# Performance work log

Hardware: AMD Instinct MI355X
Metric: run time of the kernel (lower is better)

The kernel has to match this reference:

```python
import jax, jax.numpy as jnp
import numpy as np

EPS = 1e-12  # tf.math.l2_normalize epsilon

def _l2norm(x):
    # normalize over last axis, matching K.l2_normalize semantics
    sq = jnp.sum(x * x, axis=-1, keepdims=True)
    return x * jax.lax.rsqrt(jnp.maximum(sq, EPS))

def setup_inputs() -> dict:
    key = jax.random.key(0)
    k1, k2, k3 = jax.random.split(key, 3)
    B, L, D, P = 16, 256, 256, 20
    sent1 = jax.random.normal(k1, (B, L, D), dtype=jnp.float32)
    sent2 = jax.random.normal(k2, (B, L, D), dtype=jnp.float32)
    # glorot_uniform for shape (P, D)
    limit = np.sqrt(6.0 / (P + D)).astype(np.float32)
    kernel = jax.random.uniform(k3, (P, D), minval=-limit, maxval=limit, dtype=jnp.float32)
    return {"sent1": sent1, "sent2": sent2, "kernel": kernel}

def reference(sent1, sent2, kernel):
    # sent1: [B,L1,D], sent2: [B,L2,D], kernel: [P,D]
    v1 = _l2norm(sent1[:, :, None, :] * kernel)  # [B,L1,P,D]
    v2 = _l2norm(sent2[:, :, None, :] * kernel)  # [B,L2,P,D]
    # per-perspective cosine similarity matrix: [B,L1,L2,P]
    cos = jnp.einsum('blpd,bmpd->blmp', v1, v2)
    # max over the other sentence's positions (L2) -> [B,L1,P]
    return jnp.max(cos, axis=2)
```

## Files before the change

### kernel.cpp

```cpp
#include <hip/hip_runtime.h>
#include <hip/hip_bf16.h>


#define B_DIM 16
#define L_DIM 256
#define D_DIM 256
#define P_DIM 20
#define EPS 1e-12f
#define LDP 264

typedef __attribute__((ext_vector_type(8))) __bf16 bf16x8;
typedef __attribute__((ext_vector_type(4))) float f32x4;

__device__ __forceinline__ unsigned short f2bf(float x) {
  unsigned int u = __float_as_uint(x);
  u += 0x7fffu + ((u >> 16) & 1u);
  return (unsigned short)(u >> 16);
}

__global__ __launch_bounds__(256)
void prep2(const float* __restrict__ s1, const float* __restrict__ s2,
           const float* __restrict__ kg,
           float* __restrict__ rn1, float* __restrict__ rn2,
           unsigned short* __restrict__ s1bf, unsigned short* __restrict__ s2bf) {
  __shared__ __align__(16) unsigned short QA[32 * LDP];
  __shared__ __align__(16) unsigned short QB[32 * LDP];
  const int tid = threadIdx.x, lane = tid & 63, wave = tid >> 6;
  const int lr = lane & 15, q = lane >> 4;
  const int sent = blockIdx.x & 1, t = blockIdx.x >> 1;
  const int r0 = t * 32, b = r0 >> 8;
  const float* src = sent ? s2 : s1;
  unsigned short* sbf = sent ? s2bf : s1bf;
  float* rn = sent ? rn2 : rn1;

  #pragma unroll
  for (int i = 0; i < 8; ++i) {
    const int row = i * 4 + wave;
    float4 sv = *(const float4*)(src + (size_t)(r0 + row) * D_DIM + lane * 4);
    unsigned int c0 = ((unsigned int)f2bf(sv.y) << 16) | f2bf(sv.x);
    unsigned int c1 = ((unsigned int)f2bf(sv.w) << 16) | f2bf(sv.z);
    *(uint2*)&sbf[(size_t)(r0 + row) * D_DIM + lane * 4] = make_uint2(c0, c1);
    unsigned int q0 = ((unsigned int)f2bf(sv.y * sv.y) << 16) | f2bf(sv.x * sv.x);
    unsigned int q1 = ((unsigned int)f2bf(sv.w * sv.w) << 16) | f2bf(sv.z * sv.z);
    *(uint2*)&QA[row * LDP + lane * 4] = make_uint2(q0, q1);
  }
  #pragma unroll
  for (int j = 0; j < 5; ++j) {
    const int row = wave * 5 + j;
    float4 kv = *(const float4*)(kg + row * D_DIM + lane * 4);
    unsigned int c0 = ((unsigned int)f2bf(kv.y * kv.y) << 16) | f2bf(kv.x * kv.x);
    unsigned int c1 = ((unsigned int)f2bf(kv.w * kv.w) << 16) | f2bf(kv.z * kv.z);
    *(uint2*)&QB[row * LDP + lane * 4] = make_uint2(c0, c1);
  }
  __syncthreads();

  const int mt = wave & 1, nt = wave >> 1;
  f32x4 acc = {0.f, 0.f, 0.f, 0.f};
  #pragma unroll
  for (int ks = 0; ks < 8; ++ks) {
    const int cc = ks * 4 + q;
    bf16x8 a  = *(const bf16x8*)&QA[(mt * 16 + lr) * LDP + cc * 8];
    bf16x8 bb = *(const bf16x8*)&QB[(nt * 16 + lr) * LDP + cc * 8];
    acc = __builtin_amdgcn_mfma_f32_16x16x32_bf16(a, bb, acc, 0, 0, 0);
  }
  const int p = nt * 16 + lr;
  if (p < P_DIM) {
    #pragma unroll
    for (int r = 0; r < 4; ++r) {
      const int l = (r0 & 255) + mt * 16 + q * 4 + r;
      rn[((size_t)b * P_DIM + p) * L_DIM + l] = rsqrtf(fmaxf(acc[r], EPS));
    }
  }
}

__global__ __launch_bounds__(512, 1)
void mpm_main(const unsigned short* __restrict__ s1bf,
              const unsigned short* __restrict__ s2bf,
              const float* __restrict__ kg, const float* __restrict__ rn1,
              const float* __restrict__ rn2, float* __restrict__ outg) {
  __shared__ __align__(16) unsigned short X2[256 * 256];
  __shared__ __align__(16) unsigned short X1[64 * 256];
  float* WoutF = (float*)X1;

  const int tid = threadIdx.x, lane = tid & 63, wave = tid >> 6;
  const int lr = lane & 15, q = lane >> 4;
  const int bid = blockIdx.x;
  const int pgi = bid & 3, lt = (bid >> 2) & 3, b = bid >> 4;
  const int l0 = lt * 64;

  {
    const unsigned short* s2b = s2bf + (size_t)b * L_DIM * D_DIM;
    #pragma unroll
    for (int j = 0; j < 16; ++j) {
      int g = j * 512 + tid;
      int r = g >> 5, pr = g & 31;
      int c = pr ^ (r & 31);
      __builtin_amdgcn_global_load_lds(
          (const __attribute__((address_space(1))) void*)(s2b + r * 256 + c * 8),
          (__attribute__((address_space(3))) void*)(X2 + (size_t)g * 8), 16, 0, 0);
    }
  }

  uint2 s1r[8];
  {
    const unsigned short* s1b = s1bf + ((size_t)b * L_DIM + l0) * D_DIM;
    #pragma unroll
    for (int i = 0; i < 8; ++i)
      s1r[i] = *(const uint2*)(s1b + (size_t)(i * 8 + wave) * D_DIM + lane * 4);
  }

  const int mrow0 = wave * 32 + lr,  mrow1 = wave * 32 + 16 + lr;
  const int mkey0 = mrow0 & 31,      mkey1 = mrow1 & 31;

  #pragma unroll 1
  for (int pp = 0; pp < 5; ++pp) {
    const int p = pgi * 5 + pp;
    __syncthreads();

    {
      float4 kv = *(const float4*)(kg + p * D_DIM + lane * 4);
      const float k0 = kv.x * kv.x, k1 = kv.y * kv.y, k2 = kv.z * kv.z, k3 = kv.w * kv.w;
      const float* rn1b = rn1 + ((size_t)b * P_DIM + p) * L_DIM + l0;
      #pragma unroll
      for (int i = 0; i < 8; ++i) {
        const int row = i * 8 + wave;
        const float rv = rn1b[row];
        float x0 = __uint_as_float(s1r[i].x << 16)          * k0 * rv;
        float x1 = __uint_as_float(s1r[i].x & 0xffff0000u)  * k1 * rv;
        float x2 = __uint_as_float(s1r[i].y << 16)          * k2 * rv;
        float x3 = __uint_as_float(s1r[i].y & 0xffff0000u)  * k3 * rv;
        unsigned int c0 = ((unsigned int)f2bf(x1) << 16) | f2bf(x0);
        unsigned int c1 = ((unsigned int)f2bf(x3) << 16) | f2bf(x2);
        *(uint2*)&X1[row * 256 + (((lane >> 1) ^ (row & 31)) << 3) + ((lane & 1) << 2)] =
            make_uint2(c0, c1);
      }
    }
    __syncthreads();

    f32x4 acc[2][4];
    #pragma unroll
    for (int mi = 0; mi < 2; ++mi)
      #pragma unroll
      for (int li = 0; li < 4; ++li) acc[mi][li] = (f32x4){0.f, 0.f, 0.f, 0.f};

    #pragma unroll
    for (int ks = 0; ks < 8; ++ks) {
      const int cc = ks * 4 + q;
      bf16x8 a0 = *(const bf16x8*)&X2[mrow0 * 256 + ((cc ^ mkey0) << 3)];
      bf16x8 a1 = *(const bf16x8*)&X2[mrow1 * 256 + ((cc ^ mkey1) << 3)];
      bf16x8 bb[4];
      #pragma unroll
      for (int li = 0; li < 4; ++li) {
        const int l = li * 16 + lr;
        bb[li] = *(const bf16x8*)&X1[l * 256 + ((cc ^ (l & 31)) << 3)];
      }
      #pragma unroll
      for (int li = 0; li < 4; ++li) {
        acc[0][li] = __builtin_amdgcn_mfma_f32_16x16x32_bf16(a0, bb[li], acc[0][li], 0, 0, 0);
        acc[1][li] = __builtin_amdgcn_mfma_f32_16x16x32_bf16(a1, bb[li], acc[1][li], 0, 0, 0);
      }
    }

    float4 r20, r21;
    {
      const float* rn2b = rn2 + ((size_t)b * P_DIM + p) * L_DIM + wave * 32;
      r20 = *(const float4*)(rn2b + q * 4);
      r21 = *(const float4*)(rn2b + 16 + q * 4);
    }
    float v[4];
    #pragma unroll
    for (int li = 0; li < 4; ++li) {
      float t = -3.4e38f;
      t = fmaxf(t, fmaxf(acc[0][li][0] * r20.x, acc[1][li][0] * r21.x));
      t = fmaxf(t, fmaxf(acc[0][li][1] * r20.y, acc[1][li][1] * r21.y));
      t = fmaxf(t, fmaxf(acc[0][li][2] * r20.z, acc[1][li][2] * r21.z));
      t = fmaxf(t, fmaxf(acc[0][li][3] * r20.w, acc[1][li][3] * r21.w));
      t = fmaxf(t, __shfl_xor(t, 16));
      t = fmaxf(t, __shfl_xor(t, 32));
      v[li] = t;
    }

    __syncthreads();
    if (q == 0) {
      #pragma unroll
      for (int li = 0; li < 4; ++li) WoutF[wave * 64 + li * 16 + lr] = v[li];
    }
    __syncthreads();
    if (tid < 64) {
      float o = WoutF[tid];
      #pragma unroll
      for (int w = 1; w < 8; ++w) o = fmaxf(o, WoutF[w * 64 + tid]);
      outg[((size_t)b * L_DIM + (l0 + tid)) * P_DIM + p] = o;
    }
  }
}

extern "C" void kernel_launch(void* const* d_in, const int* in_sizes, int n_in,
                              void* d_out, int out_size, void* d_ws, size_t ws_size,
                              hipStream_t stream) {
  const float* s1 = (const float*)d_in[0];
  const float* s2 = (const float*)d_in[1];
  const float* kg = (const float*)d_in[2];
  float* out = (float*)d_out;

  float* rn1 = (float*)d_ws;
  float* rn2 = rn1 + (size_t)B_DIM * P_DIM * L_DIM;
  unsigned short* s2bf = (unsigned short*)(rn2 + (size_t)B_DIM * P_DIM * L_DIM);
  unsigned short* s1bf = s2bf + (size_t)B_DIM * L_DIM * D_DIM;

  prep2<<<dim3(256), dim3(256), 0, stream>>>(s1, s2, kg, rn1, rn2, s1bf, s2bf);
  mpm_main<<<dim3(256), dim3(512), 0, stream>>>(s1bf, s2bf, kg, rn1, rn2, out);
}
```

Baseline: 82.63 us.

## Fuse norm-precompute prep kernel into main kernel and apply rn1 after max

Removes the separate prep kernel and its workspace round trip. Each block now converts fp32 s1/s2 to bf16 itself and computes per-perspective inverse norms via MFMA for its own rows and for all s2 rows of its batch. The s1 norm scaling moves out of the operand and is applied after the max, which is valid because the norm is positive. This adds redundant s2 conversion and norm work per block and replaces async LDS loads with register staging. It also remaps block IDs to spread batches.

```diff
diff --git a/kernel.cpp b/kernel.cpp
--- a/kernel.cpp
+++ b/kernel.cpp
@@ -7,10 +7,11 @@
 #define D_DIM 256
 #define P_DIM 20
 #define EPS 1e-12f
-#define LDP 264
 
 typedef __attribute__((ext_vector_type(8))) __bf16 bf16x8;
 typedef __attribute__((ext_vector_type(4))) float f32x4;
+
+union BV { bf16x8 v; unsigned short u[8]; };
 
 __device__ __forceinline__ unsigned short f2bf(float x) {
   unsigned int u = __float_as_uint(x);
@@ -18,99 +19,129 @@
   return (unsigned short)(u >> 16);
 }
 
-__global__ __launch_bounds__(256)
-void prep2(const float* __restrict__ s1, const float* __restrict__ s2,
-           const float* __restrict__ kg,
-           float* __restrict__ rn1, float* __restrict__ rn2,
-           unsigned short* __restrict__ s1bf, unsigned short* __restrict__ s2bf) {
-  __shared__ __align__(16) unsigned short QA[32 * LDP];
-  __shared__ __align__(16) unsigned short QB[32 * LDP];
+__global__ __launch_bounds__(512, 1)
+void mpm_fused(const float* __restrict__ s1, const float* __restrict__ s2,
+               const float* __restrict__ kg, float* __restrict__ outg) {
+  __shared__ __align__(16) unsigned short X2[256 * 256];
+  __shared__ __align__(16) unsigned short X1[64 * 256];
+  float* WoutF  = (float*)X1;
+  float* Rn1col = ((float*)X1) + 512;
+
   const int tid = threadIdx.x, lane = tid & 63, wave = tid >> 6;
   const int lr = lane & 15, q = lane >> 4;
-  const int sent = blockIdx.x & 1, t = blockIdx.x >> 1;
-  const int r0 = t * 32, b = r0 >> 8;
-  const float* src = sent ? s2 : s1;
-  unsigned short* sbf = sent ? s2bf : s1bf;
-  float* rn = sent ? rn2 : rn1;
-
-  #pragma unroll
-  for (int i = 0; i < 8; ++i) {
-    const int row = i * 4 + wave;
-    float4 sv = *(const float4*)(src + (size_t)(r0 + row) * D_DIM + lane * 4);
-    unsigned int c0 = ((unsigned int)f2bf(sv.y) << 16) | f2bf(sv.x);
-    unsigned int c1 = ((unsigned int)f2bf(sv.w) << 16) | f2bf(sv.z);
-    *(uint2*)&sbf[(size_t)(r0 + row) * D_DIM + lane * 4] = make_uint2(c0, c1);
-    unsigned int q0 = ((unsigned int)f2bf(sv.y * sv.y) << 16) | f2bf(sv.x * sv.x);
-    unsigned int q1 = ((unsigned int)f2bf(sv.w * sv.w) << 16) | f2bf(sv.z * sv.z);
-    *(uint2*)&QA[row * LDP + lane * 4] = make_uint2(q0, q1);
-  }
-  #pragma unroll
-  for (int j = 0; j < 5; ++j) {
-    const int row = wave * 5 + j;
-    float4 kv = *(const float4*)(kg + row * D_DIM + lane * 4);
-    unsigned int c0 = ((unsigned int)f2bf(kv.y * kv.y) << 16) | f2bf(kv.x * kv.x);
-    unsigned int c1 = ((unsigned int)f2bf(kv.w * kv.w) << 16) | f2bf(kv.z * kv.z);
-    *(uint2*)&QB[row * LDP + lane * 4] = make_uint2(c0, c1);
-  }
-  __syncthreads();
-
-  const int mt = wave & 1, nt = wave >> 1;
-  f32x4 acc = {0.f, 0.f, 0.f, 0.f};
-  #pragma unroll
-  for (int ks = 0; ks < 8; ++ks) {
-    const int cc = ks * 4 + q;
-    bf16x8 a  = *(const bf16x8*)&QA[(mt * 16 + lr) * LDP + cc * 8];
-    bf16x8 bb = *(const bf16x8*)&QB[(nt * 16 + lr) * LDP + cc * 8];
-    acc = __builtin_amdgcn_mfma_f32_16x16x32_bf16(a, bb, acc, 0, 0, 0);
-  }
-  const int p = nt * 16 + lr;
-  if (p < P_DIM) {
-    #pragma unroll
-    for (int r = 0; r < 4; ++r) {
-      const int l = (r0 & 255) + mt * 16 + q * 4 + r;
-      rn[((size_t)b * P_DIM + p) * L_DIM + l] = rsqrtf(fmaxf(acc[r], EPS));
-    }
-  }
-}
-
-__global__ __launch_bounds__(512, 1)
-void mpm_main(const unsigned short* __restrict__ s1bf,
-              const unsigned short* __restrict__ s2bf,
-              const float* __restrict__ kg, const float* __restrict__ rn1,
-              const float* __restrict__ rn2, float* __restrict__ outg) {
-  __shared__ __align__(16) unsigned short X2[256 * 256];
-  __shared__ __align__(16) unsigned short X1[64 * 256];
-  float* WoutF = (float*)X1;
-
-  const int tid = threadIdx.x, lane = tid & 63, wave = tid >> 6;
-  const int lr = lane & 15, q = lane >> 4;
-  const int bid = blockIdx.x;
+
+  const int bid = (int)((blockIdx.x >> 3) + (blockIdx.x & 7) * 32);
   const int pgi = bid & 3, lt = (bid >> 2) & 3, b = bid >> 4;
   const int l0 = lt * 64;
 
+  float4 s1f[8];
   {
-    const unsigned short* s2b = s2bf + (size_t)b * L_DIM * D_DIM;
-    #pragma unroll
-    for (int j = 0; j < 16; ++j) {
-      int g = j * 512 + tid;
-      int r = g >> 5, pr = g & 31;
-      int c = pr ^ (r & 31);
-      __builtin_amdgcn_global_load_lds(
-          (const __attribute__((address_space(1))) void*)(s2b + r * 256 + c * 8),
-          (__attribute__((address_space(3))) void*)(X2 + (size_t)g * 8), 16, 0, 0);
-    }
+    const float* s1b = s1 + ((size_t)b * L_DIM + l0) * D_DIM;
+    #pragma unroll
+    for (int i = 0; i < 8; ++i)
+      s1f[i] = *(const float4*)(s1b + (size_t)(i * 8 + wave) * D_DIM + lane * 4);
+  }
+
+  const float* s2b = s2 + (size_t)b * L_DIM * D_DIM;
+  float4 sv[8];
+  #pragma unroll
+  for (int i = 0; i < 8; ++i)
+    sv[i] = *(const float4*)(s2b + (size_t)(i * 8 + wave) * D_DIM + lane * 4);
+
+  bf16x8 bk2[8];
+  {
+    const bool ok = (lr < 5);
+    const float* kr = kg + (size_t)(pgi * 5 + lr) * D_DIM + q * 8;
+    #pragma unroll
+    for (int ks = 0; ks < 8; ++ks) {
+      BV t;
+      if (ok) {
+        float4 a = *(const float4*)(kr + ks * 32);
+        float4 c = *(const float4*)(kr + ks * 32 + 4);
+        t.u[0] = f2bf(a.x * a.x); t.u[1] = f2bf(a.y * a.y);
+        t.u[2] = f2bf(a.z * a.z); t.u[3] = f2bf(a.w * a.w);
+        t.u[4] = f2bf(c.x * c.x); t.u[5] = f2bf(c.y * c.y);
+        t.u[6] = f2bf(c.z * c.z); t.u[7] = f2bf(c.w * c.w);
+      } else {
+        #pragma unroll
+        for (int e = 0; e < 8; ++e) t.u[e] = 0;
+      }
+      bk2[ks] = t.v;
+    }
+  }
+
+  f32x4 an2[2] = {{0.f, 0.f, 0.f, 0.f}, {0.f, 0.f, 0.f, 0.f}};
+  #pragma unroll
+  for (int g = 0; g < 4; ++g) {
+    #pragma unroll
+    for (int i = 0; i < 8; ++i) {
+      const int r = g * 64 + i * 8 + wave, rl = r & 63;
+      const int colsw = (((lane >> 1) ^ (r & 31)) << 3) + ((lane & 1) << 2);
+      unsigned int c0 = ((unsigned int)f2bf(sv[i].y) << 16) | f2bf(sv[i].x);
+      unsigned int c1 = ((unsigned int)f2bf(sv[i].w) << 16) | f2bf(sv[i].z);
+      *(uint2*)&X2[r * 256 + colsw] = make_uint2(c0, c1);
+      unsigned int q0 = ((unsigned int)f2bf(sv[i].y * sv[i].y) << 16) | f2bf(sv[i].x * sv[i].x);
+      unsigned int q1 = ((unsigned int)f2bf(sv[i].w * sv[i].w) << 16) | f2bf(sv[i].z * sv[i].z);
+      *(uint2*)&X1[rl * 256 + colsw] = make_uint2(q0, q1);
+    }
+    if (g < 3) {
+      #pragma unroll
+      for (int i = 0; i < 8; ++i)
+        sv[i] = *(const float4*)(s2b + (size_t)((g + 1) * 64 + i * 8 + wave) * D_DIM + lane * 4);
+    }
+    __syncthreads();
+    if ((wave >> 1) == g) {
+      #pragma unroll
+      for (int t = 0; t < 2; ++t) {
+        const int row = ((wave & 1) * 2 + t) * 16 + lr;
+        #pragma unroll
+        for (int ks = 0; ks < 8; ++ks) {
+          const int cc = ks * 4 + q;
+          bf16x8 a = *(const bf16x8*)&X1[row * 256 + ((cc ^ (row & 31)) << 3)];
+          an2[t] = __builtin_amdgcn_mfma_f32_16x16x32_bf16(a, bk2[ks], an2[t], 0, 0, 0);
+        }
+      }
+    }
+    __syncthreads();
   }
 
   uint2 s1r[8];
-  {
-    const unsigned short* s1b = s1bf + ((size_t)b * L_DIM + l0) * D_DIM;
-    #pragma unroll
-    for (int i = 0; i < 8; ++i)
-      s1r[i] = *(const uint2*)(s1b + (size_t)(i * 8 + wave) * D_DIM + lane * 4);
-  }
-
-  const int mrow0 = wave * 32 + lr,  mrow1 = wave * 32 + 16 + lr;
-  const int mkey0 = mrow0 & 31,      mkey1 = mrow1 & 31;
+  #pragma unroll
+  for (int i = 0; i < 8; ++i) {
+    const int row = i * 8 + wave;
+    const int colsw = (((lane >> 1) ^ (row & 31)) << 3) + ((lane & 1) << 2);
+    unsigned int c0 = ((unsigned int)f2bf(s1f[i].y) << 16) | f2bf(s1f[i].x);
+    unsigned int c1 = ((unsigned int)f2bf(s1f[i].w) << 16) | f2bf(s1f[i].z);
+    s1r[i] = make_uint2(c0, c1);
+    unsigned int q0 = ((unsigned int)f2bf(s1f[i].y * s1f[i].y) << 16) | f2bf(s1f[i].x * s1f[i].x);
+    unsigned int q1 = ((unsigned int)f2bf(s1f[i].w * s1f[i].w) << 16) | f2bf(s1f[i].z * s1f[i].z);
+    *(uint2*)&X1[row * 256 + colsw] = make_uint2(q0, q1);
+  }
+  __syncthreads();
+  float rn1v[4][4];
+  if (wave == 0) {
+    #pragma unroll
+    for (int t = 0; t < 4; ++t) {
+      f32x4 a4 = {0.f, 0.f, 0.f, 0.f};
+      const int row = t * 16 + lr;
+      #pragma unroll
+      for (int ks = 0; ks < 8; ++ks) {
+        const int cc = ks * 4 + q;
+        bf16x8 a = *(const bf16x8*)&X1[row * 256 + ((cc ^ (row & 31)) << 3)];
+        a4 = __builtin_amdgcn_mfma_f32_16x16x32_bf16(a, bk2[ks], a4, 0, 0, 0);
+      }
+      #pragma unroll
+      for (int r = 0; r < 4; ++r) rn1v[t][r] = rsqrtf(fmaxf(a4[r], EPS));
+    }
+  }
+  float rn2v[2][4];
+  #pragma unroll
+  for (int t = 0; t < 2; ++t)
+    #pragma unroll
+    for (int r = 0; r < 4; ++r) rn2v[t][r] = rsqrtf(fmaxf(an2[t][r], EPS));
+
+  const int mrow0 = wave * 32 + lr, mrow1 = wave * 32 + 16 + lr;
+  const int mkey0 = mrow0 & 31,     mkey1 = mrow1 & 31;
 
   #pragma unroll 1
   for (int pp = 0; pp < 5; ++pp) {
@@ -118,17 +149,15 @@
     __syncthreads();
 
     {
-      float4 kv = *(const float4*)(kg + p * D_DIM + lane * 4);
+      float4 kv = *(const float4*)(kg + (size_t)p * D_DIM + lane * 4);
       const float k0 = kv.x * kv.x, k1 = kv.y * kv.y, k2 = kv.z * kv.z, k3 = kv.w * kv.w;
-      const float* rn1b = rn1 + ((size_t)b * P_DIM + p) * L_DIM + l0;
       #pragma unroll
       for (int i = 0; i < 8; ++i) {
         const int row = i * 8 + wave;
-        const float rv = rn1b[row];
-        float x0 = __uint_as_float(s1r[i].x << 16)          * k0 * rv;
-        float x1 = __uint_as_float(s1r[i].x & 0xffff0000u)  * k1 * rv;
-        float x2 = __uint_as_float(s1r[i].y << 16)          * k2 * rv;
-        float x3 = __uint_as_float(s1r[i].y & 0xffff0000u)  * k3 * rv;
+        float x0 = __uint_as_float(s1r[i].x << 16)         * k0;
+        float x1 = __uint_as_float(s1r[i].x & 0xffff0000u) * k1;
+        float x2 = __uint_as_float(s1r[i].y << 16)         * k2;
+        float x3 = __uint_as_float(s1r[i].y & 0xffff0000u) * k3;
         unsigned int c0 = ((unsigned int)f2bf(x1) << 16) | f2bf(x0);
         unsigned int c1 = ((unsigned int)f2bf(x3) << 16) | f2bf(x2);
         *(uint2*)&X1[row * 256 + (((lane >> 1) ^ (row & 31)) << 3) + ((lane & 1) << 2)] =
@@ -161,20 +190,19 @@
       }
     }
 
-    float4 r20, r21;
-    {
-      const float* rn2b = rn2 + ((size_t)b * P_DIM + p) * L_DIM + wave * 32;
-      r20 = *(const float4*)(rn2b + q * 4);
-      r21 = *(const float4*)(rn2b + 16 + q * 4);
-    }
+    float r2[2][4];
+    #pragma unroll
+    for (int t = 0; t < 2; ++t)
+      #pragma unroll
+      for (int r = 0; r < 4; ++r) r2[t][r] = __shfl(rn2v[t][r], q * 16 + pp);
+
     float v[4];
     #pragma unroll
     for (int li = 0; li < 4; ++li) {
       float t = -3.4e38f;
-      t = fmaxf(t, fmaxf(acc[0][li][0] * r20.x, acc[1][li][0] * r21.x));
-      t = fmaxf(t, fmaxf(acc[0][li][1] * r20.y, acc[1][li][1] * r21.y));
-      t = fmaxf(t, fmaxf(acc[0][li][2] * r20.z, acc[1][li][2] * r21.z));
-      t = fmaxf(t, fmaxf(acc[0][li][3] * r20.w, acc[1][li][3] * r21.w));
+      #pragma unroll
+      for (int r = 0; r < 4; ++r)
+        t = fmaxf(t, fmaxf(acc[0][li][r] * r2[0][r], acc[1][li][r] * r2[1][r]));
       t = fmaxf(t, __shfl_xor(t, 16));
       t = fmaxf(t, __shfl_xor(t, 32));
       v[li] = t;
@@ -185,12 +213,18 @@
       #pragma unroll
       for (int li = 0; li < 4; ++li) WoutF[wave * 64 + li * 16 + lr] = v[li];
     }
+    if (wave == 0 && lr == pp) {
+      #pragma unroll
+      for (int t = 0; t < 4; ++t)
+        #pragma unroll
+        for (int r = 0; r < 4; ++r) Rn1col[t * 16 + q * 4 + r] = rn1v[t][r];
+    }
     __syncthreads();
     if (tid < 64) {
       float o = WoutF[tid];
       #pragma unroll
       for (int w = 1; w < 8; ++w) o = fmaxf(o, WoutF[w * 64 + tid]);
-      outg[((size_t)b * L_DIM + (l0 + tid)) * P_DIM + p] = o;
+      outg[((size_t)b * L_DIM + (l0 + tid)) * P_DIM + p] = o * Rn1col[tid];
     }
   }
 }
@@ -198,16 +232,11 @@
 extern "C" void kernel_launch(void* const* d_in, const int* in_sizes, int n_in,
                               void* d_out, int out_size, void* d_ws, size_t ws_size,
                               hipStream_t stream) {
+  (void)in_sizes; (void)n_in; (void)out_size; (void)d_ws; (void)ws_size;
   const float* s1 = (const float*)d_in[0];
   const float* s2 = (const float*)d_in[1];
   const float* kg = (const float*)d_in[2];
   float* out = (float*)d_out;
 
-  float* rn1 = (float*)d_ws;
-  float* rn2 = rn1 + (size_t)B_DIM * P_DIM * L_DIM;
-  unsigned short* s2bf = (unsigned short*)(rn2 + (size_t)B_DIM * P_DIM * L_DIM);
-  unsigned short* s1bf = s2bf + (size_t)B_DIM * L_DIM * D_DIM;
-
-  prep2<<<dim3(256), dim3(256), 0, stream>>>(s1, s2, kg, rn1, rn2, s1bf, s2bf);
-  mpm_main<<<dim3(256), dim3(512), 0, stream>>>(s1bf, s2bf, kg, rn1, rn2, out);
+  mpm_fused<<<dim3(256), dim3(512), 0, stream>>>(s1, s2, kg, out);
 }
```

New measurement: 82.98 us. Within noise of the previous version (+0.4%).

## Hold sentence-2 tiles in registers, halve L1 tile, raise occupancy

Applied to the files above, without the earlier changes.

Sentence-2 MFMA fragments now load straight from global memory into registers instead of being staged in a 128KB LDS buffer. This cuts LDS use to about 16KB and lets several blocks share a CU (launch bounds now 4). The L1 tile drops from 64 to 32 rows, which doubles the grid to 512 blocks, and block indices are remapped to spread batches across the grid. The rn1 scaling moves from per-element prescaling to a single multiply after the max, which is valid because rn1 is positive, and one barrier per iteration is removed. The trade-offs are each block reloading its s2 fragments and higher register pressure, with the 64-VGPR s2 fragment array possibly limiting occupancy.

```diff
diff --git a/kernel.cpp b/kernel.cpp
--- a/kernel.cpp
+++ b/kernel.cpp
@@ -73,91 +73,82 @@
   }
 }
 
-__global__ __launch_bounds__(512, 1)
+__global__ __launch_bounds__(512, 4)
 void mpm_main(const unsigned short* __restrict__ s1bf,
               const unsigned short* __restrict__ s2bf,
               const float* __restrict__ kg, const float* __restrict__ rn1,
               const float* __restrict__ rn2, float* __restrict__ outg) {
-  __shared__ __align__(16) unsigned short X2[256 * 256];
-  __shared__ __align__(16) unsigned short X1[64 * 256];
-  float* WoutF = (float*)X1;
+  __shared__ __align__(16) unsigned short X1[32 * 256];
+  __shared__ float Wout[8 * 32];
 
   const int tid = threadIdx.x, lane = tid & 63, wave = tid >> 6;
   const int lr = lane & 15, q = lane >> 4;
-  const int bid = blockIdx.x;
-  const int pgi = bid & 3, lt = (bid >> 2) & 3, b = bid >> 4;
-  const int l0 = lt * 64;
-
+
+  const int bid = (int)((blockIdx.x >> 3) + (blockIdx.x & 7) * 64);
+  const int pgi = bid & 3, lt = (bid >> 2) & 7, b = bid >> 5;
+  const int l0 = lt * 32;
+
+  bf16x8 af[2][8];
   {
-    const unsigned short* s2b = s2bf + (size_t)b * L_DIM * D_DIM;
-    #pragma unroll
-    for (int j = 0; j < 16; ++j) {
-      int g = j * 512 + tid;
-      int r = g >> 5, pr = g & 31;
-      int c = pr ^ (r & 31);
-      __builtin_amdgcn_global_load_lds(
-          (const __attribute__((address_space(1))) void*)(s2b + r * 256 + c * 8),
-          (__attribute__((address_space(3))) void*)(X2 + (size_t)g * 8), 16, 0, 0);
-    }
-  }
-
-  uint2 s1r[8];
+    const unsigned short* s2b2 = s2bf + (size_t)b * (L_DIM * D_DIM);
+    #pragma unroll
+    for (int mi = 0; mi < 2; ++mi) {
+      const unsigned short* rp = s2b2 + (size_t)(wave * 32 + mi * 16 + lr) * D_DIM + q * 8;
+      #pragma unroll
+      for (int ks = 0; ks < 8; ++ks)
+        af[mi][ks] = *(const bf16x8*)(rp + ks * 32);
+    }
+  }
+
+  uint2 s1r[4];
   {
-    const unsigned short* s1b = s1bf + ((size_t)b * L_DIM + l0) * D_DIM;
-    #pragma unroll
-    for (int i = 0; i < 8; ++i)
-      s1r[i] = *(const uint2*)(s1b + (size_t)(i * 8 + wave) * D_DIM + lane * 4);
-  }
-
-  const int mrow0 = wave * 32 + lr,  mrow1 = wave * 32 + 16 + lr;
-  const int mkey0 = mrow0 & 31,      mkey1 = mrow1 & 31;
+    const unsigned short* s1b2 = s1bf + ((size_t)b * L_DIM + l0) * D_DIM;
+    #pragma unroll
+    for (int i = 0; i < 4; ++i)
+      s1r[i] = *(const uint2*)(s1b2 + (size_t)(i * 8 + wave) * D_DIM + lane * 4);
+  }
 
   #pragma unroll 1
   for (int pp = 0; pp < 5; ++pp) {
     const int p = pgi * 5 + pp;
-    __syncthreads();
 
     {
-      float4 kv = *(const float4*)(kg + p * D_DIM + lane * 4);
+      float4 kv = *(const float4*)(kg + (size_t)p * D_DIM + lane * 4);
       const float k0 = kv.x * kv.x, k1 = kv.y * kv.y, k2 = kv.z * kv.z, k3 = kv.w * kv.w;
-      const float* rn1b = rn1 + ((size_t)b * P_DIM + p) * L_DIM + l0;
-      #pragma unroll
-      for (int i = 0; i < 8; ++i) {
+      #pragma unroll
+      for (int i = 0; i < 4; ++i) {
         const int row = i * 8 + wave;
-        const float rv = rn1b[row];
-        float x0 = __uint_as_float(s1r[i].x << 16)          * k0 * rv;
-        float x1 = __uint_as_float(s1r[i].x & 0xffff0000u)  * k1 * rv;
-        float x2 = __uint_as_float(s1r[i].y << 16)          * k2 * rv;
-        float x3 = __uint_as_float(s1r[i].y & 0xffff0000u)  * k3 * rv;
+        float x0 = __uint_as_float(s1r[i].x << 16)         * k0;
+        float x1 = __uint_as_float(s1r[i].x & 0xffff0000u) * k1;
+        float x2 = __uint_as_float(s1r[i].y << 16)         * k2;
+        float x3 = __uint_as_float(s1r[i].y & 0xffff0000u) * k3;
         unsigned int c0 = ((unsigned int)f2bf(x1) << 16) | f2bf(x0);
         unsigned int c1 = ((unsigned int)f2bf(x3) << 16) | f2bf(x2);
-        *(uint2*)&X1[row * 256 + (((lane >> 1) ^ (row & 31)) << 3) + ((lane & 1) << 2)] =
+        *(uint2*)&X1[row * 256 + (((lane >> 1) ^ row) << 3) + ((lane & 1) << 2)] =
             make_uint2(c0, c1);
       }
     }
     __syncthreads();
 
-    f32x4 acc[2][4];
+    f32x4 acc[2][2];
     #pragma unroll
     for (int mi = 0; mi < 2; ++mi)
       #pragma unroll
-      for (int li = 0; li < 4; ++li) acc[mi][li] = (f32x4){0.f, 0.f, 0.f, 0.f};
+      for (int li = 0; li < 2; ++li) acc[mi][li] = (f32x4){0.f, 0.f, 0.f, 0.f};
 
     #pragma unroll
     for (int ks = 0; ks < 8; ++ks) {
       const int cc = ks * 4 + q;
-      bf16x8 a0 = *(const bf16x8*)&X2[mrow0 * 256 + ((cc ^ mkey0) << 3)];
-      bf16x8 a1 = *(const bf16x8*)&X2[mrow1 * 256 + ((cc ^ mkey1) << 3)];
-      bf16x8 bb[4];
-      #pragma unroll
-      for (int li = 0; li < 4; ++li) {
+      bf16x8 bb[2];
+      #pragma unroll
+      for (int li = 0; li < 2; ++li) {
         const int l = li * 16 + lr;
-        bb[li] = *(const bf16x8*)&X1[l * 256 + ((cc ^ (l & 31)) << 3)];
+        bb[li] = *(const bf16x8*)&X1[l * 256 + ((cc ^ l) << 3)];
       }
       #pragma unroll
-      for (int li = 0; li < 4; ++li) {
-        acc[0][li] = __builtin_amdgcn_mfma_f32_16x16x32_bf16(a0, bb[li], acc[0][li], 0, 0, 0);
-        acc[1][li] = __builtin_amdgcn_mfma_f32_16x16x32_bf16(a1, bb[li], acc[1][li], 0, 0, 0);
+      for (int li = 0; li < 2; ++li) {
+        acc[0][li] = __builtin_amdgcn_mfma_f32_16x16x32_bf16(af[0][ks], bb[li], acc[0][li], 0, 0, 0);
+        acc[1][li] = __builtin_amdgcn_mfma_f32_16x16x32_bf16(af[1][ks], bb[li], acc[1][li], 0, 0, 0);
       }
     }
 
@@ -167,9 +158,9 @@
       r20 = *(const float4*)(rn2b + q * 4);
       r21 = *(const float4*)(rn2b + 16 + q * 4);
     }
-    float v[4];
-    #pragma unroll
-    for (int li = 0; li < 4; ++li) {
+    float v[2];
+    #pragma unroll
+    for (int li = 0; li < 2; ++li) {
       float t = -3.4e38f;
       t = fmaxf(t, fmaxf(acc[0][li][0] * r20.x, acc[1][li][0] * r21.x));
       t = fmaxf(t, fmaxf(acc[0][li][1] * r20.y, acc[1][li][1] * r21.y));
@@ -179,18 +170,17 @@
       t = fmaxf(t, __shfl_xor(t, 32));
       v[li] = t;
     }
-
+    if (q == 0) {
+      #pragma unroll
+      for (int li = 0; li < 2; ++li) Wout[wave * 32 + li * 16 + lr] = v[li];
+    }
     __syncthreads();
-    if (q == 0) {
-      #pragma unroll
-      for (int li = 0; li < 4; ++li) WoutF[wave * 64 + li * 16 + lr] = v[li];
-    }
-    __syncthreads();
-    if (tid < 64) {
-      float o = WoutF[tid];
-      #pragma unroll
-      for (int w = 1; w < 8; ++w) o = fmaxf(o, WoutF[w * 64 + tid]);
-      outg[((size_t)b * L_DIM + (l0 + tid)) * P_DIM + p] = o;
+    if (tid < 32) {
+      float o = Wout[tid];
+      #pragma unroll
+      for (int w = 1; w < 8; ++w) o = fmaxf(o, Wout[w * 32 + tid]);
+      const float r1 = rn1[((size_t)b * P_DIM + p) * L_DIM + l0 + tid];
+      outg[((size_t)b * L_DIM + (l0 + tid)) * P_DIM + p] = o * r1;
     }
   }
 }
@@ -198,6 +188,7 @@
 extern "C" void kernel_launch(void* const* d_in, const int* in_sizes, int n_in,
                               void* d_out, int out_size, void* d_ws, size_t ws_size,
                               hipStream_t stream) {
+  (void)in_sizes; (void)n_in; (void)out_size; (void)ws_size;
   const float* s1 = (const float*)d_in[0];
   const float* s2 = (const float*)d_in[1];
   const float* kg = (const float*)d_in[2];
@@ -209,5 +200,5 @@
   unsigned short* s1bf = s2bf + (size_t)B_DIM * L_DIM * D_DIM;
 
   prep2<<<dim3(256), dim3(256), 0, stream>>>(s1, s2, kg, rn1, rn2, s1bf, s2bf);
-  mpm_main<<<dim3(256), dim3(512), 0, stream>>>(s1bf, s2bf, kg, rn1, rn2, out);
-}
+  mpm_main<<<dim3(512), dim3(512), 0, stream>>>(s1bf, s2bf, kg, rn1, rn2, out);
+}
```

After: 88.89 us. 7.6% more time.
